# Kernel optimization log

Measured on AMD Instinct MI355X. Metric: run time of the kernel, lower is better.

The kernel has to match this reference:

```python
import jax, jax.numpy as jnp
import numpy as np

D_MODEL = 1024
N_HEADS = 16
HEAD_DIM = D_MODEL // N_HEADS
B, S = 2, 2048


def setup_inputs() -> dict:
    key = jax.random.key(0)
    ks = jax.random.split(key, 12)
    std = 1.0 / np.sqrt(D_MODEL)
    mk = lambda k: (jax.random.normal(k, (D_MODEL, D_MODEL), jnp.float32) * std)
    return {
        "query": jax.random.normal(ks[0], (B, S, D_MODEL), jnp.float32),
        "key": jax.random.normal(ks[1], (B, S, D_MODEL), jnp.float32),
        "value": jax.random.normal(ks[2], (B, S, D_MODEL), jnp.float32),
        "Wq": mk(ks[3]), "bq": jnp.zeros((D_MODEL,), jnp.float32),
        "Wk": mk(ks[4]), "bk": jnp.zeros((D_MODEL,), jnp.float32),
        "Wv": mk(ks[5]), "bv": jnp.zeros((D_MODEL,), jnp.float32),
        "Wo": mk(ks[6]), "bo": jnp.zeros((D_MODEL,), jnp.float32),
    }


def reference(query, key, value, Wq, bq, Wk, bk, Wv, bv, Wo, bo):
    b, s, d = query.shape
    # Linear projections (torch Linear: x @ W.T + b)
    q = query @ Wq.T + bq
    k = key @ Wk.T + bk
    v = value @ Wv.T + bv
    # [B, H, S, Dh]
    split = lambda x: x.reshape(b, -1, N_HEADS, HEAD_DIM).transpose(0, 2, 1, 3)
    qh, kh, vh = split(q), split(k), split(v)
    scores = jnp.einsum("bhqd,bhkd->bhqk", qh, kh) / jnp.sqrt(
        jnp.asarray(HEAD_DIM, qh.dtype))
    attn = jax.nn.softmax(scores, axis=-1)
    out = jnp.einsum("bhqk,bhkd->bhqd", attn, vh)
    out = out.transpose(0, 2, 1, 3).reshape(b, -1, N_HEADS * HEAD_DIM)
    return out @ Wo.T + bo
```

## Files before the change

### kernel.cpp

```cpp
#include <hip/hip_runtime.h>
#include <hip/hip_bf16.h>


typedef short bf16x8 __attribute__((ext_vector_type(8)));
typedef short bf16x4 __attribute__((ext_vector_type(4)));
typedef float f32x4  __attribute__((ext_vector_type(4)));

constexpr size_t NE = (size_t)4096 * 1024;
constexpr size_t NW = (size_t)1024 * 1024;

#if __has_builtin(__builtin_amdgcn_exp2f)
#define EXP2(x) __builtin_amdgcn_exp2f(x)
#else
#define EXP2(x) exp2f(x)
#endif

__device__ __forceinline__ short f2bf(float f) {
  __hip_bfloat16 h = __float2bfloat16(f);
  return *reinterpret_cast<short*>(&h);
}

__device__ __forceinline__ void cp16(const short* g, short* l) {
  __builtin_amdgcn_global_load_lds(
      (const __attribute__((address_space(1))) void*)g,
      (__attribute__((address_space(3))) void*)l, 16, 0, 0);
}

__global__ __launch_bounds__(256) void cvt_kernel(
    const float* q, const float* k, const float* v,
    const float* Wq, const float* Wk, const float* Wv, const float* Wo,
    short* qb, short* kb, short* vb,
    short* Wqb, short* Wkb, short* Wvb, short* Wob) {
  const int y = blockIdx.y;
  const float* s; short* d;
  if (y < 12) {
    const int t = y >> 2;
    const size_t off = (size_t)(y & 3) << 20;
    s = (t == 0 ? q : (t == 1 ? k : v)) + off;
    d = (t == 0 ? qb : (t == 1 ? kb : vb)) + off;
  } else {
    s = (y == 12 ? Wq : (y == 13 ? Wk : (y == 14 ? Wv : Wo)));
    d = (y == 12 ? Wqb : (y == 13 ? Wkb : (y == 14 ? Wvb : Wob)));
  }
  size_t i = (size_t)blockIdx.x * 256 + threadIdx.x;
  float4 val = ((const float4*)s)[i];
  bf16x4 o;
  o[0] = f2bf(val.x); o[1] = f2bf(val.y); o[2] = f2bf(val.z); o[3] = f2bf(val.w);
  ((bf16x4*)d)[i] = o;
}

__global__ __launch_bounds__(256) void gemm_qkv(
    const short* __restrict__ A0, const short* __restrict__ A1, const short* __restrict__ A2,
    const short* __restrict__ W0, const short* __restrict__ W1, const short* __restrict__ W2,
    const float* __restrict__ b0, const float* __restrict__ b1, const float* __restrict__ b2,
    short* __restrict__ C0, short* __restrict__ C1, short* __restrict__ Cv) {
  __shared__ short As[2][128 * 32];
  __shared__ short Bs[2][128 * 32];
  const int which = blockIdx.y;
  const short* A    = which == 0 ? A0 : (which == 1 ? A1 : A2);
  const short* W    = which == 0 ? W0 : (which == 1 ? W1 : W2);
  const float* bias = which == 0 ? b0 : (which == 1 ? b1 : b2);
  const float scale = which == 0 ? 0.18033688011112042f : 1.0f;

  const int tid  = threadIdx.x;
  const int bm   = (int)blockIdx.x >> 3;
  const int bn   = (int)blockIdx.x & 7;
  const int lane = tid & 63, wid = tid >> 6;
  const int g = lane >> 4, l15 = lane & 15;
  const int wm = (wid >> 1) * 64, wn = (wid & 1) * 64;

  const short* Ag = A + (size_t)(bm * 128 + (tid >> 2)) * 1024 + (tid & 3) * 8;
  const short* Wg = W + (size_t)(bn * 128 + (tid >> 2)) * 1024 + (tid & 3) * 8;
  const int wofs = wid * 512;

  f32x4 acc[4][4];
#pragma unroll
  for (int i = 0; i < 4; ++i)
#pragma unroll
    for (int j = 0; j < 4; ++j) acc[i][j] = (f32x4){0.f, 0.f, 0.f, 0.f};

  for (int k0 = 0; k0 < 1024; k0 += 64) {
    __syncthreads();
#pragma unroll
    for (int p = 0; p < 2; ++p) {
      const int kk = k0 + p * 32;
      cp16(Ag + kk,             As[p] + wofs);
      cp16(Ag + 64 * 1024 + kk, As[p] + wofs + 2048);
      cp16(Wg + kk,             Bs[p] + wofs);
      cp16(Wg + 64 * 1024 + kk, Bs[p] + wofs + 2048);
    }
    __syncthreads();

#pragma unroll
    for (int p = 0; p < 2; ++p) {
      bf16x8 af[4], bf[4];
#pragma unroll
      for (int mt = 0; mt < 4; ++mt)
        af[mt] = *(const bf16x8*)&As[p][(wm + mt * 16 + l15) * 32 + g * 8];
#pragma unroll
      for (int nt = 0; nt < 4; ++nt)
        bf[nt] = *(const bf16x8*)&Bs[p][(wn + nt * 16 + l15) * 32 + g * 8];
#pragma unroll
      for (int mt = 0; mt < 4; ++mt)
#pragma unroll
        for (int nt = 0; nt < 4; ++nt)
          acc[mt][nt] = __builtin_amdgcn_mfma_f32_16x16x32_bf16(
              af[mt], bf[nt], acc[mt][nt], 0, 0, 0);
    }
  }

  const int col0 = bn * 128 + wn;
  if (which < 2) {
    short* C = which == 0 ? C0 : C1;
#pragma unroll
    for (int nt = 0; nt < 4; ++nt) {
      const int col = col0 + nt * 16 + l15;
      const float bb = bias[col];
#pragma unroll
      for (int mt = 0; mt < 4; ++mt) {
        const int m0 = bm * 128 + wm + mt * 16 + g * 4;
#pragma unroll
        for (int r = 0; r < 4; ++r)
          C[(size_t)(m0 + r) * 1024 + col] = f2bf((acc[mt][nt][r] + bb) * scale);
      }
    }
  } else {
#pragma unroll
    for (int nt = 0; nt < 4; ++nt) {
      const int col = col0 + nt * 16 + l15;
      const int h = col >> 6, dh = col & 63;
      const float bb = bias[col];
#pragma unroll
      for (int mt = 0; mt < 4; ++mt) {
        const int m0 = bm * 128 + wm + mt * 16 + g * 4;
        const int bb_ = m0 >> 11, s0 = m0 & 2047;
        bf16x4 o;
#pragma unroll
        for (int r = 0; r < 4; ++r) o[r] = f2bf(acc[mt][nt][r] + bb);
        *(bf16x4*)&Cv[(((size_t)bb_ * 16 + h) * 64 + dh) * 2048 + s0] = o;
      }
    }
  }
}

__global__ __launch_bounds__(256) void gemm_out(
    const short* __restrict__ A, const short* __restrict__ W,
    const float* __restrict__ bias, float* __restrict__ C) {
  __shared__ short As[2][64 * 32];
  __shared__ short Bs[2][128 * 32];
  const int tid  = threadIdx.x;
  const int bm   = (int)blockIdx.x >> 3;
  const int bn   = (int)blockIdx.x & 7;
  const int lane = tid & 63, wid = tid >> 6;
  const int g = lane >> 4, l15 = lane & 15;
  const int wm = (wid >> 1) * 32, wn = (wid & 1) * 64;

  const short* Ag = A + (size_t)(bm * 64 + (tid >> 2)) * 1024 + (tid & 3) * 8;
  const short* Wg = W + (size_t)(bn * 128 + (tid >> 2)) * 1024 + (tid & 3) * 8;
  const int wofs = wid * 512;

  f32x4 acc[2][4];
#pragma unroll
  for (int i = 0; i < 2; ++i)
#pragma unroll
    for (int j = 0; j < 4; ++j) acc[i][j] = (f32x4){0.f, 0.f, 0.f, 0.f};

  for (int k0 = 0; k0 < 1024; k0 += 64) {
    __syncthreads();
#pragma unroll
    for (int p = 0; p < 2; ++p) {
      const int kk = k0 + p * 32;
      cp16(Ag + kk,             As[p] + tid * 8 - tid * 8 + wofs);
      cp16(Wg + kk,             Bs[p] + wofs);
      cp16(Wg + 64 * 1024 + kk, Bs[p] + wofs + 2048);
    }
    __syncthreads();

#pragma unroll
    for (int p = 0; p < 2; ++p) {
      bf16x8 af[2], bf[4];
#pragma unroll
      for (int mt = 0; mt < 2; ++mt)
        af[mt] = *(const bf16x8*)&As[p][(wm + mt * 16 + l15) * 32 + g * 8];
#pragma unroll
      for (int nt = 0; nt < 4; ++nt)
        bf[nt] = *(const bf16x8*)&Bs[p][(wn + nt * 16 + l15) * 32 + g * 8];
#pragma unroll
      for (int mt = 0; mt < 2; ++mt)
#pragma unroll
        for (int nt = 0; nt < 4; ++nt)
          acc[mt][nt] = __builtin_amdgcn_mfma_f32_16x16x32_bf16(
              af[mt], bf[nt], acc[mt][nt], 0, 0, 0);
    }
  }

  const int col0 = bn * 128 + wn;
#pragma unroll
  for (int nt = 0; nt < 4; ++nt) {
    const int col = col0 + nt * 16 + l15;
    const float bb = bias[col];
#pragma unroll
    for (int mt = 0; mt < 2; ++mt) {
      const int m0 = bm * 64 + wm + mt * 16 + g * 4;
#pragma unroll
      for (int r = 0; r < 4; ++r)
        C[(size_t)(m0 + r) * 1024 + col] = acc[mt][nt][r] + bb;
    }
  }
}

__global__ __launch_bounds__(256) void attn_kernel(
    const short* __restrict__ Q, const short* __restrict__ K,
    const short* __restrict__ Vg, short* __restrict__ O) {
  __shared__ short Kt[64][72];
  __shared__ short Vt[64][72];
  __shared__ short Pt[4][32][72];

  const int tid  = threadIdx.x;
  const int qt   = (int)blockIdx.x & 15;
  const int bh   = (int)blockIdx.x >> 4;
  const int b    = bh >> 4, h = bh & 15;
  const int lane = tid & 63, wid = tid >> 6;
  const int g = lane >> 4, l15 = lane & 15;

  const int q0 = qt * 128 + wid * 32;
  bf16x8 qf[2][2];
#pragma unroll
  for (int mt = 0; mt < 2; ++mt) {
    const size_t base = (size_t)(b * 2048 + q0 + mt * 16 + l15) * 1024 + h * 64;
    qf[mt][0] = *(const bf16x8*)(Q + base + g * 8);
    qf[mt][1] = *(const bf16x8*)(Q + base + 32 + g * 8);
  }

  f32x4 o_acc[2][4];
#pragma unroll
  for (int i = 0; i < 2; ++i)
#pragma unroll
    for (int j = 0; j < 4; ++j) o_acc[i][j] = (f32x4){0.f, 0.f, 0.f, 0.f};
  float l_i[2][4];
#pragma unroll
  for (int i = 0; i < 2; ++i)
#pragma unroll
    for (int r = 0; r < 4; ++r) l_i[i][r] = 0.f;

  const int srow = tid >> 2, sch = tid & 3;
  const short* Kbase = K + (size_t)(b * 2048) * 1024 + h * 64 + sch * 8;
  const short* Vbase = Vg + (size_t)((b * 16 + h) * 64 + srow) * 2048 + sch * 8;

  bf16x8 nk0, nk1, nv0, nv1;
  {
    const short* krow = Kbase + (size_t)srow * 1024;
    nk0 = *(const bf16x8*)(krow);
    nk1 = *(const bf16x8*)(krow + 32);
    nv0 = *(const bf16x8*)(Vbase);
    nv1 = *(const bf16x8*)(Vbase + 32);
  }

  for (int kt = 0; kt < 32; ++kt) {
    __syncthreads();
    *(bf16x8*)&Kt[srow][sch * 8]      = nk0;
    *(bf16x8*)&Kt[srow][sch * 8 + 32] = nk1;
    *(bf16x8*)&Vt[srow][sch * 8]      = nv0;
    *(bf16x8*)&Vt[srow][sch * 8 + 32] = nv1;
    __syncthreads();

    if (kt < 31) {
      const short* krow = Kbase + (size_t)((kt + 1) * 64 + srow) * 1024;
      nk0 = *(const bf16x8*)(krow);
      nk1 = *(const bf16x8*)(krow + 32);
      nv0 = *(const bf16x8*)(Vbase + (kt + 1) * 64);
      nv1 = *(const bf16x8*)(Vbase + (kt + 1) * 64 + 32);
    }

    f32x4 sv[2][4];
#pragma unroll
    for (int nt = 0; nt < 4; ++nt) {
      bf16x8 kf0 = *(const bf16x8*)&Kt[nt * 16 + l15][g * 8];
      bf16x8 kf1 = *(const bf16x8*)&Kt[nt * 16 + l15][32 + g * 8];
#pragma unroll
      for (int mt = 0; mt < 2; ++mt) {
        f32x4 z = (f32x4){0.f, 0.f, 0.f, 0.f};
        z = __builtin_amdgcn_mfma_f32_16x16x32_bf16(qf[mt][0], kf0, z, 0, 0, 0);
        z = __builtin_amdgcn_mfma_f32_16x16x32_bf16(qf[mt][1], kf1, z, 0, 0, 0);
        sv[mt][nt] = z;
      }
    }

#pragma unroll
    for (int mt = 0; mt < 2; ++mt)
#pragma unroll
      for (int r = 0; r < 4; ++r) {
        float p0 = EXP2(sv[mt][0][r]);
        float p1 = EXP2(sv[mt][1][r]);
        float p2 = EXP2(sv[mt][2][r]);
        float p3 = EXP2(sv[mt][3][r]);
        l_i[mt][r] += (p0 + p1) + (p2 + p3);
        const int pr = mt * 16 + g * 4 + r;
        Pt[wid][pr][l15]      = f2bf(p0);
        Pt[wid][pr][16 + l15] = f2bf(p1);
        Pt[wid][pr][32 + l15] = f2bf(p2);
        Pt[wid][pr][48 + l15] = f2bf(p3);
      }

    bf16x8 pf[2][2];
#pragma unroll
    for (int mt = 0; mt < 2; ++mt) {
      pf[mt][0] = *(const bf16x8*)&Pt[wid][mt * 16 + l15][g * 8];
      pf[mt][1] = *(const bf16x8*)&Pt[wid][mt * 16 + l15][32 + g * 8];
    }
#pragma unroll
    for (int nt = 0; nt < 4; ++nt) {
      bf16x8 vf0 = *(const bf16x8*)&Vt[nt * 16 + l15][g * 8];
      bf16x8 vf1 = *(const bf16x8*)&Vt[nt * 16 + l15][32 + g * 8];
#pragma unroll
      for (int mt = 0; mt < 2; ++mt) {
        o_acc[mt][nt] = __builtin_amdgcn_mfma_f32_16x16x32_bf16(
            pf[mt][0], vf0, o_acc[mt][nt], 0, 0, 0);
        o_acc[mt][nt] = __builtin_amdgcn_mfma_f32_16x16x32_bf16(
            pf[mt][1], vf1, o_acc[mt][nt], 0, 0, 0);
      }
    }
  }

#pragma unroll
  for (int mt = 0; mt < 2; ++mt)
#pragma unroll
    for (int r = 0; r < 4; ++r) {
      float l = l_i[mt][r];
#pragma unroll
      for (int off = 1; off < 16; off <<= 1) l += __shfl_xor(l, off, 64);
      const float inv = 1.0f / l;
      const int row = q0 + mt * 16 + g * 4 + r;
      const size_t base = (size_t)(b * 2048 + row) * 1024 + h * 64;
#pragma unroll
      for (int nt = 0; nt < 4; ++nt)
        O[base + nt * 16 + l15] = f2bf(o_acc[mt][nt][r] * inv);
    }
}

extern "C" void kernel_launch(void* const* d_in, const int* in_sizes, int n_in,
                              void* d_out, int out_size, void* d_ws, size_t ws_size,
                              hipStream_t stream) {
  (void)in_sizes; (void)n_in; (void)out_size; (void)ws_size;
  const float* q  = (const float*)d_in[0];
  const float* k  = (const float*)d_in[1];
  const float* v  = (const float*)d_in[2];
  const float* Wq = (const float*)d_in[3];
  const float* bq = (const float*)d_in[4];
  const float* Wk = (const float*)d_in[5];
  const float* bk = (const float*)d_in[6];
  const float* Wv = (const float*)d_in[7];
  const float* bv = (const float*)d_in[8];
  const float* Wo = (const float*)d_in[9];
  const float* bo = (const float*)d_in[10];
  float* out = (float*)d_out;

  short* qb  = (short*)d_ws;
  short* kb  = qb + NE;
  short* vb  = kb + NE;
  short* Wqb = vb + NE;
  short* Wkb = Wqb + NW;
  short* Wvb = Wkb + NW;
  short* Wob = Wvb + NW;
  short* Qw  = Wob + NW;
  short* Kw  = Qw + NE;
  short* Vtg = Kw + NE;
  short* Ob  = qb;

  cvt_kernel<<<dim3(1024, 16), 256, 0, stream>>>(q, k, v, Wq, Wk, Wv, Wo,
                                                 qb, kb, vb, Wqb, Wkb, Wvb, Wob);
  gemm_qkv<<<dim3(256, 3), 256, 0, stream>>>(qb, kb, vb, Wqb, Wkb, Wvb,
                                             bq, bk, bv, Qw, Kw, Vtg);
  attn_kernel<<<512, 256, 0, stream>>>(Qw, Kw, Vtg, Ob);
  gemm_out<<<512, 256, 0, stream>>>(Ob, Wob, bo, out);
}
```

Baseline: 241.7 us.

## Double-buffer LDS tiles in GEMMs and attention to overlap loads with MFMA

The two projection GEMMs previously loaded both K-halves into LDS, hit a barrier, then computed, so global loads and MFMA work never overlapped. They now prefetch the next 32-wide K slice into the alternate LDS buffer while computing on the current one, with one barrier per step. The attention kernel gets double-buffered K/V tiles indexed by iteration parity, which removes one barrier per key tile. This costs extra LDS in attention and relies on the barrier waiting for the async LDS loads to land.

```diff
diff --git a/kernel.cpp b/kernel.cpp
--- a/kernel.cpp
+++ b/kernel.cpp
@@ -79,34 +79,34 @@
 #pragma unroll
     for (int j = 0; j < 4; ++j) acc[i][j] = (f32x4){0.f, 0.f, 0.f, 0.f};
 
-  for (int k0 = 0; k0 < 1024; k0 += 64) {
+  cp16(Ag,             As[0] + wofs);
+  cp16(Ag + 64 * 1024, As[0] + wofs + 2048);
+  cp16(Wg,             Bs[0] + wofs);
+  cp16(Wg + 64 * 1024, Bs[0] + wofs + 2048);
+
+  for (int r = 0; r < 32; ++r) {
+    const int cur = r & 1;
     __syncthreads();
-#pragma unroll
-    for (int p = 0; p < 2; ++p) {
-      const int kk = k0 + p * 32;
-      cp16(Ag + kk,             As[p] + wofs);
-      cp16(Ag + 64 * 1024 + kk, As[p] + wofs + 2048);
-      cp16(Wg + kk,             Bs[p] + wofs);
-      cp16(Wg + 64 * 1024 + kk, Bs[p] + wofs + 2048);
-    }
-    __syncthreads();
-
-#pragma unroll
-    for (int p = 0; p < 2; ++p) {
-      bf16x8 af[4], bf[4];
-#pragma unroll
-      for (int mt = 0; mt < 4; ++mt)
-        af[mt] = *(const bf16x8*)&As[p][(wm + mt * 16 + l15) * 32 + g * 8];
+    if (r < 31) {
+      const int kk = (r + 1) * 32, nxt = cur ^ 1;
+      cp16(Ag + kk,             As[nxt] + wofs);
+      cp16(Ag + 64 * 1024 + kk, As[nxt] + wofs + 2048);
+      cp16(Wg + kk,             Bs[nxt] + wofs);
+      cp16(Wg + 64 * 1024 + kk, Bs[nxt] + wofs + 2048);
+    }
+    bf16x8 af[4], bf[4];
+#pragma unroll
+    for (int mt = 0; mt < 4; ++mt)
+      af[mt] = *(const bf16x8*)&As[cur][(wm + mt * 16 + l15) * 32 + g * 8];
+#pragma unroll
+    for (int nt = 0; nt < 4; ++nt)
+      bf[nt] = *(const bf16x8*)&Bs[cur][(wn + nt * 16 + l15) * 32 + g * 8];
+#pragma unroll
+    for (int mt = 0; mt < 4; ++mt)
 #pragma unroll
       for (int nt = 0; nt < 4; ++nt)
-        bf[nt] = *(const bf16x8*)&Bs[p][(wn + nt * 16 + l15) * 32 + g * 8];
-#pragma unroll
-      for (int mt = 0; mt < 4; ++mt)
-#pragma unroll
-        for (int nt = 0; nt < 4; ++nt)
-          acc[mt][nt] = __builtin_amdgcn_mfma_f32_16x16x32_bf16(
-              af[mt], bf[nt], acc[mt][nt], 0, 0, 0);
-    }
+        acc[mt][nt] = __builtin_amdgcn_mfma_f32_16x16x32_bf16(
+            af[mt], bf[nt], acc[mt][nt], 0, 0, 0);
   }
 
   const int col0 = bn * 128 + wn;
@@ -165,33 +165,32 @@
 #pragma unroll
     for (int j = 0; j < 4; ++j) acc[i][j] = (f32x4){0.f, 0.f, 0.f, 0.f};
 
-  for (int k0 = 0; k0 < 1024; k0 += 64) {
+  cp16(Ag,             As[0] + wofs);
+  cp16(Wg,             Bs[0] + wofs);
+  cp16(Wg + 64 * 1024, Bs[0] + wofs + 2048);
+
+  for (int r = 0; r < 32; ++r) {
+    const int cur = r & 1;
     __syncthreads();
-#pragma unroll
-    for (int p = 0; p < 2; ++p) {
-      const int kk = k0 + p * 32;
-      cp16(Ag + kk,             As[p] + tid * 8 - tid * 8 + wofs);
-      cp16(Wg + kk,             Bs[p] + wofs);
-      cp16(Wg + 64 * 1024 + kk, Bs[p] + wofs + 2048);
-    }
-    __syncthreads();
-
-#pragma unroll
-    for (int p = 0; p < 2; ++p) {
-      bf16x8 af[2], bf[4];
-#pragma unroll
-      for (int mt = 0; mt < 2; ++mt)
-        af[mt] = *(const bf16x8*)&As[p][(wm + mt * 16 + l15) * 32 + g * 8];
+    if (r < 31) {
+      const int kk = (r + 1) * 32, nxt = cur ^ 1;
+      cp16(Ag + kk,             As[nxt] + wofs);
+      cp16(Wg + kk,             Bs[nxt] + wofs);
+      cp16(Wg + 64 * 1024 + kk, Bs[nxt] + wofs + 2048);
+    }
+    bf16x8 af[2], bf[4];
+#pragma unroll
+    for (int mt = 0; mt < 2; ++mt)
+      af[mt] = *(const bf16x8*)&As[cur][(wm + mt * 16 + l15) * 32 + g * 8];
+#pragma unroll
+    for (int nt = 0; nt < 4; ++nt)
+      bf[nt] = *(const bf16x8*)&Bs[cur][(wn + nt * 16 + l15) * 32 + g * 8];
+#pragma unroll
+    for (int mt = 0; mt < 2; ++mt)
 #pragma unroll
       for (int nt = 0; nt < 4; ++nt)
-        bf[nt] = *(const bf16x8*)&Bs[p][(wn + nt * 16 + l15) * 32 + g * 8];
-#pragma unroll
-      for (int mt = 0; mt < 2; ++mt)
-#pragma unroll
-        for (int nt = 0; nt < 4; ++nt)
-          acc[mt][nt] = __builtin_amdgcn_mfma_f32_16x16x32_bf16(
-              af[mt], bf[nt], acc[mt][nt], 0, 0, 0);
-    }
+        acc[mt][nt] = __builtin_amdgcn_mfma_f32_16x16x32_bf16(
+            af[mt], bf[nt], acc[mt][nt], 0, 0, 0);
   }
 
   const int col0 = bn * 128 + wn;
@@ -212,8 +211,8 @@
 __global__ __launch_bounds__(256) void attn_kernel(
     const short* __restrict__ Q, const short* __restrict__ K,
     const short* __restrict__ Vg, short* __restrict__ O) {
-  __shared__ short Kt[64][72];
-  __shared__ short Vt[64][72];
+  __shared__ short Kt[2][64][72];
+  __shared__ short Vt[2][64][72];
   __shared__ short Pt[4][32][72];
 
   const int tid  = threadIdx.x;
@@ -257,11 +256,11 @@
   }
 
   for (int kt = 0; kt < 32; ++kt) {
-    __syncthreads();
-    *(bf16x8*)&Kt[srow][sch * 8]      = nk0;
-    *(bf16x8*)&Kt[srow][sch * 8 + 32] = nk1;
-    *(bf16x8*)&Vt[srow][sch * 8]      = nv0;
-    *(bf16x8*)&Vt[srow][sch * 8 + 32] = nv1;
+    const int cur = kt & 1;
+    *(bf16x8*)&Kt[cur][srow][sch * 8]      = nk0;
+    *(bf16x8*)&Kt[cur][srow][sch * 8 + 32] = nk1;
+    *(bf16x8*)&Vt[cur][srow][sch * 8]      = nv0;
+    *(bf16x8*)&Vt[cur][srow][sch * 8 + 32] = nv1;
     __syncthreads();
 
     if (kt < 31) {
@@ -275,8 +274,8 @@
     f32x4 sv[2][4];
 #pragma unroll
     for (int nt = 0; nt < 4; ++nt) {
-      bf16x8 kf0 = *(const bf16x8*)&Kt[nt * 16 + l15][g * 8];
-      bf16x8 kf1 = *(const bf16x8*)&Kt[nt * 16 + l15][32 + g * 8];
+      bf16x8 kf0 = *(const bf16x8*)&Kt[cur][nt * 16 + l15][g * 8];
+      bf16x8 kf1 = *(const bf16x8*)&Kt[cur][nt * 16 + l15][32 + g * 8];
 #pragma unroll
       for (int mt = 0; mt < 2; ++mt) {
         f32x4 z = (f32x4){0.f, 0.f, 0.f, 0.f};
@@ -310,8 +309,8 @@
     }
 #pragma unroll
     for (int nt = 0; nt < 4; ++nt) {
-      bf16x8 vf0 = *(const bf16x8*)&Vt[nt * 16 + l15][g * 8];
-      bf16x8 vf1 = *(const bf16x8*)&Vt[nt * 16 + l15][32 + g * 8];
+      bf16x8 vf0 = *(const bf16x8*)&Vt[cur][nt * 16 + l15][g * 8];
+      bf16x8 vf1 = *(const bf16x8*)&Vt[cur][nt * 16 + l15][32 + g * 8];
 #pragma unroll
       for (int mt = 0; mt < 2; ++mt) {
         o_acc[mt][nt] = __builtin_amdgcn_mfma_f32_16x16x32_bf16(
```

After: 248.1 us. 2.6% more time.
